# Kernel tuning notes

Hardware: AMD Instinct MI355X
Metric: run time of the kernel (lower is better)

## Reference

```python
import jax, jax.numpy as jnp
import numpy as np

N, T, D, H = 4, 2048, 512, 8
HD = D // H  # head dim = split size


def setup_inputs() -> dict:
    key = jax.random.key(0)
    k1, k2, k3, k4 = jax.random.split(key, 4)
    scale = 1.0 / np.sqrt(D)
    return {
        "query": jax.random.normal(k1, (N, T, D), dtype=jnp.float32),
        "Wk": jax.random.normal(k2, (D, D), dtype=jnp.float32) * scale,
        "Wv": jax.random.normal(k3, (D, D), dtype=jnp.float32) * scale,
        "Wo": jax.random.normal(k4, (D, D), dtype=jnp.float32) * scale,
    }


def reference(query, Wk, Wv, Wo):
    # torch.nn.Linear(x) == x @ W.T (no bias)
    querys = query                              # [N, T, D]
    keys = query @ Wk.T + query                 # residual-added keys [N, T, D]
    values = query @ Wv.T                       # [N, T, D]

    # split along feature dim into H heads, stacked on a leading head axis
    def split_heads(x):
        # [N, T, D] -> [H, N, T, HD]
        return jnp.transpose(x.reshape(N, T, H, HD), (2, 0, 1, 3))

    q = split_heads(querys)
    k = split_heads(keys)
    v = split_heads(values)

    scores = jnp.einsum("hnqd,hnkd->hnqk", q, k) / np.sqrt(HD).astype(np.float32)
    scores = jax.nn.softmax(scores, axis=3)      # [H, N, Tq, Tk]
    out = jnp.einsum("hnqk,hnkd->hnqd", scores, v)

    # concat heads back along feature dim: [H, N, T, HD] -> [N, T, D]
    out = jnp.transpose(out, (1, 2, 0, 3)).reshape(N, T, D)
    out = out @ Wo.T
    return out
```

## Files before the change

### kernel.cpp

```cpp
#include <hip/hip_runtime.h>
#include <cstdint>
#include <cstddef>

#define NB 4
#define TS 2048
#define DM 512
#define HN 8
#define HD 64

typedef __attribute__((ext_vector_type(8))) short bf16x8;
typedef __attribute__((ext_vector_type(16))) float f32x16;
typedef __attribute__((ext_vector_type(4))) float f32x4;
typedef __attribute__((ext_vector_type(4))) short short4v;
typedef __attribute__((ext_vector_type(4))) unsigned u32x4;

static __device__ __forceinline__ short f2bf(float f) {
  unsigned u = __float_as_uint(f);
  unsigned r = (u + 0x7fffu + ((u >> 16) & 1u)) >> 16;
  return (short)r;
}

static __device__ __forceinline__ float bf2f(short s) {
  return __uint_as_float(((unsigned)(unsigned short)s) << 16);
}

static __device__ __forceinline__ unsigned cvtpk(float lo, float hi) {
  unsigned r;
  asm("v_cvt_pk_bf16_f32 %0, %1, %2" : "=v"(r) : "v"(lo), "v"(hi));
  return r;
}

static __device__ __forceinline__ void plane32swap(unsigned& x, unsigned& y) {
  asm volatile("v_permlane32_swap_b32 %0, %1" : "+v"(x), "+v"(y));
}

static __device__ __forceinline__ void gload16(const void* g, void* l) {
  __builtin_amdgcn_global_load_lds(
      (const __attribute__((address_space(1))) void*)g,
      (__attribute__((address_space(3))) void*)l, 16, 0, 0);
}

#define WAIT_VM(N) asm volatile("s_waitcnt vmcnt(" #N ")" ::: "memory")
#define BAR() __builtin_amdgcn_s_barrier()

#define MFMA16(a, b, c) __builtin_amdgcn_mfma_f32_16x16x32_bf16((a), (b), (c), 0, 0, 0)
#define MFMA32(a, b, c) __builtin_amdgcn_mfma_f32_32x32x16_bf16((a), (b), (c), 0, 0, 0)

__global__ __launch_bounds__(256) void cast_all(const float* __restrict__ Q,
                                                const float* __restrict__ Wk,
                                                const float* __restrict__ Wv,
                                                const float* __restrict__ Wo,
                                                short* __restrict__ Qb,
                                                short* __restrict__ Wb) {
  int i = blockIdx.x * 256 + threadIdx.x;
  const int Q4 = (NB * TS * DM) / 4;
  const float* src;
  short* dst;
  int off;
  int which = -1;
  if (i < Q4) {
    src = Q; dst = Qb; off = i;
  } else {
    int j = i - Q4;
    which = j >> 16;
    off = j & 65535;
    src = which == 0 ? Wk : (which == 1 ? Wv : Wo);
    dst = Wb + ((size_t)which << 18);
  }
  float4 v = reinterpret_cast<const float4*>(src)[off];
  if (which == 0) {
    int e0 = off * 4;
    int row = e0 >> 9;
    int col0 = e0 & 511;
    if (row >= col0 && row < col0 + 4) {
      int c = row - col0;
      if (c == 0) v.x += 1.0f;
      else if (c == 1) v.y += 1.0f;
      else if (c == 2) v.z += 1.0f;
      else v.w += 1.0f;
    }
  }
  short4v o;
  o.x = f2bf(v.x);
  o.y = f2bf(v.y);
  o.z = f2bf(v.z);
  o.w = f2bf(v.w);
  reinterpret_cast<short4v*>(dst)[off] = o;
}

__global__ __launch_bounds__(256) void gemm_kv(const short* __restrict__ Qb,
                                               const short* __restrict__ Wkb,
                                               const short* __restrict__ Wvb,
                                               short* __restrict__ KP,
                                               short* __restrict__ VP) {
  __shared__ alignas(16) short lA[2][128 * 32];
  __shared__ alignas(16) short lK[2][64 * 32];
  __shared__ alignas(16) short lV[2][64 * 32];
  const int row0 = blockIdx.x * 128;
  const int col0d = blockIdx.y * 64;
  const int tid = threadIdx.x;
  const int lane = tid & 63;
  const int wave = tid >> 6;
  const int wr = wave >> 1, wc = wave & 1;
  const int fr = lane & 15, fk = (lane >> 4) * 8;
  const int g = lane >> 4;

  f32x4 kacc[2][4], vacc[4][2];
  const f32x4 z4 = {0.f, 0.f, 0.f, 0.f};
#pragma unroll
  for (int m = 0; m < 4; ++m)
#pragma unroll
    for (int nn = 0; nn < 2; ++nn) {
      kacc[nn][m] = z4;
      vacc[m][nn] = z4;
    }

  const int sr = tid >> 2;
  const int sc8 = (tid & 3) * 8;

#define GSTAGE(buf, kt)                                                 \
  do {                                                                  \
    gload16(&Qb[(size_t)(row0 + sr) * DM + (kt) + sc8],                 \
            (char*)&lA[(buf)][0] + (size_t)tid * 16);                   \
    gload16(&Qb[(size_t)(row0 + 64 + sr) * DM + (kt) + sc8],            \
            (char*)&lA[(buf)][0] + 4096 + (size_t)tid * 16);            \
    gload16(&Wkb[(size_t)(col0d + sr) * DM + (kt) + sc8],               \
            (char*)&lK[(buf)][0] + (size_t)tid * 16);                   \
    gload16(&Wvb[(size_t)(col0d + sr) * DM + (kt) + sc8],               \
            (char*)&lV[(buf)][0] + (size_t)tid * 16);                   \
  } while (0)

  GSTAGE(0, 0);
  __syncthreads();
  int cur = 0;
  for (int kt = 0; kt < 16; ++kt) {
    if (kt < 15) GSTAGE(cur ^ 1, (kt + 1) * 32);
    bf16x8 af[4], wk[2], wv[2];
#pragma unroll
    for (int m = 0; m < 4; ++m)
      af[m] = *reinterpret_cast<const bf16x8*>(&lA[cur][(wr * 64 + m * 16 + fr) * 32 + fk]);
#pragma unroll
    for (int nn = 0; nn < 2; ++nn) {
      wk[nn] = *reinterpret_cast<const bf16x8*>(&lK[cur][(wc * 32 + nn * 16 + fr) * 32 + fk]);
      wv[nn] = *reinterpret_cast<const bf16x8*>(&lV[cur][(wc * 32 + nn * 16 + fr) * 32 + fk]);
    }
    __builtin_amdgcn_s_setprio(1);
#pragma unroll
    for (int m = 0; m < 4; ++m)
#pragma unroll
      for (int nn = 0; nn < 2; ++nn) {
        kacc[nn][m] = MFMA16(wk[nn], af[m], kacc[nn][m]);
        vacc[m][nn] = MFMA16(af[m], wv[nn], vacc[m][nn]);
      }
    __builtin_amdgcn_s_setprio(0);
    __syncthreads();
    cur ^= 1;
  }
#undef GSTAGE

#pragma unroll
  for (int nn = 0; nn < 2; ++nn) {
#pragma unroll
    for (int m = 0; m < 4; ++m) {
      int d = col0d + wc * 32 + nn * 16 + g * 4;
      int kseq = row0 + wr * 64 + m * 16 + fr;
      int h = d >> 6, dd = d & 63;
      int n = kseq >> 11, kk = kseq & (TS - 1);
      int t = kk >> 6, H = (kk >> 5) & 1;
      int ks = (dd >> 4) & 3, hfd = (dd >> 3) & 1, jb = dd & 7;
      int slot = (kk & 31) + 32 * hfd;
      short4v pk;
#pragma unroll
      for (int i = 0; i < 4; ++i) pk[i] = f2bf(kacc[nn][m][i]);
      size_t addr = ((((size_t)(n * HN + h) * 32 + t) * 8 + H * 4 + ks) * 64 + slot) * 8 + jb;
      *reinterpret_cast<short4v*>(&KP[addr]) = pk;
    }
  }
#pragma unroll
  for (int m = 0; m < 4; ++m) {
#pragma unroll
    for (int nn = 0; nn < 2; ++nn) {
      int kseq = row0 + wr * 64 + m * 16 + g * 4;
      int d = col0d + wc * 32 + nn * 16 + fr;
      int h = d >> 6, dd = d & 63;
      int n = kseq >> 11, kk = kseq & (TS - 1);
      int t = kk >> 6, hfk = (kk >> 3) & 1, jb = kk & 7;
      int ksV = (kk >> 4) & 3, D = (dd >> 5) & 1;
      int slot = (dd & 31) + 32 * hfk;
      short4v pv;
#pragma unroll
      for (int i = 0; i < 4; ++i) pv[i] = f2bf(vacc[m][nn][i]);
      size_t addr = ((((size_t)(n * HN + h) * 32 + t) * 8 + D * 4 + ksV) * 64 + slot) * 8 + jb;
      *reinterpret_cast<short4v*>(&VP[addr]) = pv;
    }
  }
}

__global__ __launch_bounds__(256) void gemm_o(const short* __restrict__ A,
                                              const short* __restrict__ W,
                                              float* __restrict__ out0) {
  __shared__ alignas(16) short lA[2][128 * 32];
  __shared__ alignas(16) short lB[2][64 * 32];
  const int row0 = blockIdx.x * 128;
  const int col0 = blockIdx.y * 64;
  const int tid = threadIdx.x;
  const int lane = tid & 63;
  const int wave = tid >> 6;
  const int wr = wave >> 1, wc = wave & 1;
  const int fr = lane & 15, fk = (lane >> 4) * 8;

  f32x4 acc[4][2];
  const f32x4 z4 = {0.f, 0.f, 0.f, 0.f};
#pragma unroll
  for (int m = 0; m < 4; ++m)
#pragma unroll
    for (int nn = 0; nn < 2; ++nn) acc[m][nn] = z4;

  const int sr = tid >> 2;
  const int sc8 = (tid & 3) * 8;

#define GSTAGE(buf, kt)                                                \
  do {                                                                 \
    gload16(&A[(size_t)(row0 + sr) * DM + (kt) + sc8],                 \
            (char*)&lA[(buf)][0] + (size_t)tid * 16);                  \
    gload16(&A[(size_t)(row0 + 64 + sr) * DM + (kt) + sc8],            \
            (char*)&lA[(buf)][0] + 4096 + (size_t)tid * 16);           \
    gload16(&W[(size_t)(col0 + sr) * DM + (kt) + sc8],                 \
            (char*)&lB[(buf)][0] + (size_t)tid * 16);                  \
  } while (0)

  GSTAGE(0, 0);
  __syncthreads();
  int cur = 0;
  for (int kt = 0; kt < 16; ++kt) {
    if (kt < 15) GSTAGE(cur ^ 1, (kt + 1) * 32);
    bf16x8 af[4], bfr[2];
#pragma unroll
    for (int m = 0; m < 4; ++m)
      af[m] = *reinterpret_cast<const bf16x8*>(&lA[cur][(wr * 64 + m * 16 + fr) * 32 + fk]);
#pragma unroll
    for (int nn = 0; nn < 2; ++nn)
      bfr[nn] = *reinterpret_cast<const bf16x8*>(&lB[cur][(wc * 32 + nn * 16 + fr) * 32 + fk]);
    __builtin_amdgcn_s_setprio(1);
#pragma unroll
    for (int m = 0; m < 4; ++m)
#pragma unroll
      for (int nn = 0; nn < 2; ++nn) acc[m][nn] = MFMA16(af[m], bfr[nn], acc[m][nn]);
    __builtin_amdgcn_s_setprio(0);
    __syncthreads();
    cur ^= 1;
  }
#undef GSTAGE

#pragma unroll
  for (int m = 0; m < 4; ++m)
#pragma unroll
    for (int nn = 0; nn < 2; ++nn)
#pragma unroll
      for (int i = 0; i < 4; ++i) {
        int gr = row0 + wr * 64 + m * 16 + (lane >> 4) * 4 + i;
        int gc = col0 + wc * 32 + nn * 16 + fr;
        out0[(size_t)gr * DM + gc] = acc[m][nn][i];
      }
}

__global__ __launch_bounds__(512, 4) void attn(const short* __restrict__ Qb,
                                               const short* __restrict__ KP,
                                               const short* __restrict__ VP,
                                               short* __restrict__ Ob) {
  __shared__ alignas(16) short kv[2][2][2][4096];
  const int bid = blockIdx.x;
  const int blk = (bid & 7) * 64 + (bid >> 3);
  const int qt = blk & 15;
  const int nh = blk >> 4;
  const int h = nh & (HN - 1);
  const int n = nh >> 3;
  const int wv = threadIdx.x >> 6, lane = threadIdx.x & 63;
  const int grp = wv >> 2, qs = wv & 3;
  const int l31 = lane & 31, hf = lane >> 5;
  const int q0 = qt * 128 + qs * 32;
  const float SC2 = 0.18033688011f;

  bf16x8 qf[4];
  const short* qrow = Qb + (size_t)(n * TS + q0 + l31) * DM + h * HD;
#pragma unroll
  for (int ks = 0; ks < 4; ++ks) {
    bf16x8 t = *reinterpret_cast<const bf16x8*>(qrow + ks * 16 + hf * 8);
#pragma unroll
    for (int j = 0; j < 8; ++j) t[j] = f2bf(bf2f(t[j]) * SC2);
    qf[ks] = t;
  }

  f32x16 o0, o1;
#pragma unroll
  for (int r = 0; r < 16; ++r) {
    o0[r] = 0.f;
    o1[r] = 0.f;
  }
  float rs[4] = {0.f, 0.f, 0.f, 0.f};

  const int tbase = grp * 16;
  const size_t nhbase = (size_t)nh * 32 * 4096;
  const int lb = lane * 16;

#define STAGE(buf, t)                                                           \
  do {                                                                          \
    const short* kS = KP + nhbase + (size_t)(t) * 4096 + qs * 1024 + lane * 8;  \
    const short* vS = VP + nhbase + (size_t)(t) * 4096 + qs * 1024 + lane * 8;  \
    char* kb_ = (char*)&kv[grp][(buf)][0][0] + qs * 2048;                       \
    char* vb_ = (char*)&kv[grp][(buf)][1][0] + qs * 2048;                       \
    gload16(kS, kb_);                                                           \
    gload16(kS + 512, kb_ + 1024);                                              \
    gload16(vS, vb_);                                                           \
    gload16(vS + 512, vb_ + 1024);                                              \
  } while (0)

  STAGE(0, tbase);

  int cur = 0;
  for (int j = 0; j < 16; ++j) {
    if (j < 15) {
      STAGE(cur ^ 1, tbase + j + 1);
      WAIT_VM(4);
    } else {
      WAIT_VM(0);
    }
    BAR();

    const char* Kl = (const char*)&kv[grp][cur][0][0];
    const char* Vl = (const char*)&kv[grp][cur][1][0];

    f32x16 s0, s1;
#pragma unroll
    for (int r = 0; r < 16; ++r) {
      s0[r] = 0.f;
      s1[r] = 0.f;
    }
    __builtin_amdgcn_s_setprio(1);
#pragma unroll
    for (int ks = 0; ks < 4; ++ks) {
      bf16x8 ka0 = *reinterpret_cast<const bf16x8*>(Kl + ks * 1024 + lb);
      bf16x8 ka1 = *reinterpret_cast<const bf16x8*>(Kl + (4 + ks) * 1024 + lb);
      s0 = MFMA32(ka0, qf[ks], s0);
      s1 = MFMA32(ka1, qf[ks], s1);
    }
    __builtin_amdgcn_s_setprio(0);

#pragma unroll
    for (int r = 0; r < 16; ++r) {
      s0[r] = __builtin_amdgcn_exp2f(s0[r]);
      s1[r] = __builtin_amdgcn_exp2f(s1[r]);
    }
#pragma unroll
    for (int r = 0; r < 16; ++r) rs[r & 3] += s0[r] + s1[r];

    unsigned w0[4][2], w1[4][2];
#pragma unroll
    for (int c = 0; c < 4; ++c) {
      w0[c][0] = cvtpk(s0[4 * c], s0[4 * c + 1]);
      w0[c][1] = cvtpk(s0[4 * c + 2], s0[4 * c + 3]);
      w1[c][0] = cvtpk(s1[4 * c], s1[4 * c + 1]);
      w1[c][1] = cvtpk(s1[4 * c + 2], s1[4 * c + 3]);
    }

    __builtin_amdgcn_s_setprio(1);
#pragma unroll
    for (int ks = 0; ks < 4; ++ks) {
      const int ce = (ks & 1) * 2, co = ce + 1;
      unsigned xa = (ks < 2) ? w0[ce][0] : w1[ce][0];
      unsigned xb = (ks < 2) ? w0[ce][1] : w1[ce][1];
      unsigned ya = (ks < 2) ? w0[co][0] : w1[co][0];
      unsigned yb = (ks < 2) ? w0[co][1] : w1[co][1];
      plane32swap(xa, ya);
      plane32swap(xb, yb);
      u32x4 pw;
      pw.x = xa;
      pw.y = xb;
      pw.z = ya;
      pw.w = yb;
      bf16x8 pa = *reinterpret_cast<bf16x8*>(&pw);

      bf16x8 v0 = *reinterpret_cast<const bf16x8*>(Vl + ks * 1024 + lb);
      bf16x8 v1 = *reinterpret_cast<const bf16x8*>(Vl + (4 + ks) * 1024 + lb);
      o0 = MFMA32(pa, v0, o0);
      o1 = MFMA32(pa, v1, o1);
    }
    __builtin_amdgcn_s_setprio(0);

    BAR();
    cur ^= 1;
  }
#undef STAGE

  float rst = (rs[0] + rs[1]) + (rs[2] + rs[3]);
  rst += __shfl_xor(rst, 32);

  float* sp = (float*)&kv[0][0][0][0];
  const int sbase = (qs * 64 + lane) * 33;
  if (grp == 1) {
#pragma unroll
    for (int r = 0; r < 16; ++r) {
      sp[sbase + r] = o0[r];
      sp[sbase + 16 + r] = o1[r];
    }
    sp[sbase + 32] = rst;
  }
  __syncthreads();
  if (grp == 0) {
#pragma unroll
    for (int r = 0; r < 16; ++r) {
      o0[r] += sp[sbase + r];
      o1[r] += sp[sbase + 16 + r];
    }
    rst += sp[sbase + 32];
    float invv = 1.0f / rst;
#pragma unroll
    for (int r = 0; r < 16; ++r) {
      int crow = (r & 3) + 8 * (r >> 2) + 4 * hf;
      float is = __shfl(invv, crow);
      int q = q0 + crow;
      size_t base = (size_t)(n * TS + q) * DM + h * HD;
      Ob[base + l31] = f2bf(o0[r] * is);
      Ob[base + 32 + l31] = f2bf(o1[r] * is);
    }
  }
}

extern "C" void kernel_launch(void* const* d_in, const int* in_sizes, int n_in,
                              void* d_out, int out_size, void* d_ws, size_t ws_size,
                              hipStream_t stream) {
  (void)in_sizes; (void)n_in; (void)out_size; (void)ws_size;
  const float* Q = (const float*)d_in[0];
  const float* Wk = (const float*)d_in[1];
  const float* Wv = (const float*)d_in[2];
  const float* Wo = (const float*)d_in[3];

  const size_t QE = (size_t)NB * TS * DM;
  const size_t WE = (size_t)DM * DM;
  short* ws = (short*)d_ws;
  short* Qb = ws;
  short* KP = Qb + QE;
  short* VP = KP + QE;
  short* Ao = VP + QE;
  short* Wkb = Ao + QE;
  short* Wvb = Wkb + WE;
  short* Wob = Wvb + WE;

  {
    int total4 = (int)((QE + 3 * WE) / 4);
    cast_all<<<total4 / 256, 256, 0, stream>>>(Q, Wk, Wv, Wo, Qb, Wkb);
  }
  {
    dim3 g(64, 8);
    gemm_kv<<<g, 256, 0, stream>>>(Qb, Wkb, Wvb, KP, VP);
  }
  attn<<<NB * HN * (TS / 128), 512, 0, stream>>>(Qb, KP, VP, Ao);
  {
    dim3 g(64, 8);
    gemm_o<<<g, 256, 0, stream>>>(Ao, Wob, (float*)d_out);
  }
}
```

Measured before the change: 79.09 us.

## Split attention keys across four wave groups with 1024-thread blocks

The attention kernel doubles its block to 1024 threads and splits each query tile's keys across four wave groups instead of two. Each group processes 32-key tiles, and staging is divided so half the waves load K and half load V. Partial outputs are combined through LDS in two passes, one per output half, to fit the smaller shared buffer. The aim is more parallelism and latency hiding per block. The cost is a heavier cross-group reduction, extra barriers, and possible register pressure from the tighter launch bounds.

Result: slower. 303.5 us (+283.8%).

```diff
diff --git a/kernel.cpp b/kernel.cpp
--- a/kernel.cpp
+++ b/kernel.cpp
@@ -264,11 +264,11 @@
       }
 }
 
-__global__ __launch_bounds__(512, 4) void attn(const short* __restrict__ Qb,
-                                               const short* __restrict__ KP,
-                                               const short* __restrict__ VP,
-                                               short* __restrict__ Ob) {
-  __shared__ alignas(16) short kv[2][2][2][4096];
+__global__ __launch_bounds__(1024, 8) void attn(const short* __restrict__ Qb,
+                                                const short* __restrict__ KP,
+                                                const short* __restrict__ VP,
+                                                short* __restrict__ Ob) {
+  __shared__ alignas(16) short kv[4][2][2][2048];
   const int bid = blockIdx.x;
   const int blk = (bid & 7) * 64 + (bid >> 3);
   const int qt = blk & 15;
@@ -303,16 +303,22 @@
   const size_t nhbase = (size_t)nh * 32 * 4096;
   const int lb = lane * 16;
 
-#define STAGE(buf, t)                                                           \
-  do {                                                                          \
-    const short* kS = KP + nhbase + (size_t)(t) * 4096 + qs * 1024 + lane * 8;  \
-    const short* vS = VP + nhbase + (size_t)(t) * 4096 + qs * 1024 + lane * 8;  \
-    char* kb_ = (char*)&kv[grp][(buf)][0][0] + qs * 2048;                       \
-    char* vb_ = (char*)&kv[grp][(buf)][1][0] + qs * 2048;                       \
-    gload16(kS, kb_);                                                           \
-    gload16(kS + 512, kb_ + 1024);                                              \
-    gload16(vS, vb_);                                                           \
-    gload16(vS + 512, vb_ + 1024);                                              \
+#define STAGE(buf, t32)                                                           \
+  do {                                                                            \
+    if (qs < 2) {                                                                 \
+      const short* kS = KP + nhbase + (size_t)(t32) * 2048 + qs * 1024 + lane * 8;\
+      char* kb_ = (char*)&kv[grp][(buf)][0][0] + qs * 2048;                       \
+      gload16(kS, kb_);                                                           \
+      gload16(kS + 512, kb_ + 1024);                                              \
+    } else {                                                                      \
+      int D_ = qs - 2;                                                            \
+      int t64_ = (t32) >> 1, Hv_ = (t32) & 1;                                     \
+      const short* vS = VP + nhbase + (size_t)t64_ * 4096 +                       \
+                        (D_ * 4 + 2 * Hv_) * 512 + lane * 8;                      \
+      char* vb_ = (char*)&kv[grp][(buf)][1][0] + D_ * 2048;                       \
+      gload16(vS, vb_);                                                           \
+      gload16(vS + 512, vb_ + 1024);                                              \
+    }                                                                             \
   } while (0)
 
   STAGE(0, tbase);
@@ -321,7 +327,7 @@
   for (int j = 0; j < 16; ++j) {
     if (j < 15) {
       STAGE(cur ^ 1, tbase + j + 1);
-      WAIT_VM(4);
+      WAIT_VM(2);
     } else {
       WAIT_VM(0);
     }
@@ -330,47 +336,35 @@
     const char* Kl = (const char*)&kv[grp][cur][0][0];
     const char* Vl = (const char*)&kv[grp][cur][1][0];
 
-    f32x16 s0, s1;
-#pragma unroll
-    for (int r = 0; r < 16; ++r) {
-      s0[r] = 0.f;
-      s1[r] = 0.f;
-    }
+    f32x16 s;
+#pragma unroll
+    for (int r = 0; r < 16; ++r) s[r] = 0.f;
     __builtin_amdgcn_s_setprio(1);
 #pragma unroll
     for (int ks = 0; ks < 4; ++ks) {
-      bf16x8 ka0 = *reinterpret_cast<const bf16x8*>(Kl + ks * 1024 + lb);
-      bf16x8 ka1 = *reinterpret_cast<const bf16x8*>(Kl + (4 + ks) * 1024 + lb);
-      s0 = MFMA32(ka0, qf[ks], s0);
-      s1 = MFMA32(ka1, qf[ks], s1);
+      bf16x8 ka = *reinterpret_cast<const bf16x8*>(Kl + ks * 1024 + lb);
+      s = MFMA32(ka, qf[ks], s);
     }
     __builtin_amdgcn_s_setprio(0);
 
 #pragma unroll
-    for (int r = 0; r < 16; ++r) {
-      s0[r] = __builtin_amdgcn_exp2f(s0[r]);
-      s1[r] = __builtin_amdgcn_exp2f(s1[r]);
-    }
-#pragma unroll
-    for (int r = 0; r < 16; ++r) rs[r & 3] += s0[r] + s1[r];
-
-    unsigned w0[4][2], w1[4][2];
+    for (int r = 0; r < 16; ++r) s[r] = __builtin_amdgcn_exp2f(s[r]);
+#pragma unroll
+    for (int r = 0; r < 16; ++r) rs[r & 3] += s[r];
+
+    unsigned w[4][2];
 #pragma unroll
     for (int c = 0; c < 4; ++c) {
-      w0[c][0] = cvtpk(s0[4 * c], s0[4 * c + 1]);
-      w0[c][1] = cvtpk(s0[4 * c + 2], s0[4 * c + 3]);
-      w1[c][0] = cvtpk(s1[4 * c], s1[4 * c + 1]);
-      w1[c][1] = cvtpk(s1[4 * c + 2], s1[4 * c + 3]);
+      w[c][0] = cvtpk(s[4 * c], s[4 * c + 1]);
+      w[c][1] = cvtpk(s[4 * c + 2], s[4 * c + 3]);
     }
 
     __builtin_amdgcn_s_setprio(1);
 #pragma unroll
-    for (int ks = 0; ks < 4; ++ks) {
-      const int ce = (ks & 1) * 2, co = ce + 1;
-      unsigned xa = (ks < 2) ? w0[ce][0] : w1[ce][0];
-      unsigned xb = (ks < 2) ? w0[ce][1] : w1[ce][1];
-      unsigned ya = (ks < 2) ? w0[co][0] : w1[co][0];
-      unsigned yb = (ks < 2) ? w0[co][1] : w1[co][1];
+    for (int ks = 0; ks < 2; ++ks) {
+      const int ce = ks * 2, co = ce + 1;
+      unsigned xa = w[ce][0], xb = w[ce][1];
+      unsigned ya = w[co][0], yb = w[co][1];
       plane32swap(xa, ya);
       plane32swap(xb, yb);
       u32x4 pw;
@@ -381,7 +375,7 @@
       bf16x8 pa = *reinterpret_cast<bf16x8*>(&pw);
 
       bf16x8 v0 = *reinterpret_cast<const bf16x8*>(Vl + ks * 1024 + lb);
-      bf16x8 v1 = *reinterpret_cast<const bf16x8*>(Vl + (4 + ks) * 1024 + lb);
+      bf16x8 v1 = *reinterpret_cast<const bf16x8*>(Vl + 2048 + ks * 1024 + lb);
       o0 = MFMA32(pa, v0, o0);
       o1 = MFMA32(pa, v1, o1);
     }
@@ -396,23 +390,38 @@
   rst += __shfl_xor(rst, 32);
 
   float* sp = (float*)&kv[0][0][0][0];
-  const int sbase = (qs * 64 + lane) * 33;
-  if (grp == 1) {
-#pragma unroll
-    for (int r = 0; r < 16; ++r) {
-      sp[sbase + r] = o0[r];
-      sp[sbase + 16 + r] = o1[r];
-    }
-    sp[sbase + 32] = rst;
+  const int widx = (grp - 1) * 256 + qs * 64 + lane;
+  __syncthreads();
+  if (grp >= 1) {
+    int b = widx * 17;
+#pragma unroll
+    for (int r = 0; r < 16; ++r) sp[b + r] = o0[r];
+    sp[b + 16] = rst;
   }
   __syncthreads();
   if (grp == 0) {
 #pragma unroll
-    for (int r = 0; r < 16; ++r) {
-      o0[r] += sp[sbase + r];
-      o1[r] += sp[sbase + 16 + r];
-    }
-    rst += sp[sbase + 32];
+    for (int g = 1; g <= 3; ++g) {
+      int b = ((g - 1) * 256 + qs * 64 + lane) * 17;
+#pragma unroll
+      for (int r = 0; r < 16; ++r) o0[r] += sp[b + r];
+      rst += sp[b + 16];
+    }
+  }
+  __syncthreads();
+  if (grp >= 1) {
+    int b = widx * 17;
+#pragma unroll
+    for (int r = 0; r < 16; ++r) sp[b + r] = o1[r];
+  }
+  __syncthreads();
+  if (grp == 0) {
+#pragma unroll
+    for (int g = 1; g <= 3; ++g) {
+      int b = ((g - 1) * 256 + qs * 64 + lane) * 17;
+#pragma unroll
+      for (int r = 0; r < 16; ++r) o1[r] += sp[b + r];
+    }
     float invv = 1.0f / rst;
 #pragma unroll
     for (int r = 0; r < 16; ++r) {
@@ -454,7 +463,7 @@
     dim3 g(64, 8);
     gemm_kv<<<g, 256, 0, stream>>>(Qb, Wkb, Wvb, KP, VP);
   }
-  attn<<<NB * HN * (TS / 128), 512, 0, stream>>>(Qb, KP, VP, Ao);
+  attn<<<NB * HN * (TS / 128), 1024, 0, stream>>>(Qb, KP, VP, Ao);
   {
     dim3 g(64, 8);
     gemm_o<<<g, 256, 0, stream>>>(Ao, Wob, (float*)d_out);
```
